# Performance work log

Hardware: AMD Instinct MI355X
Metric: run time of the kernel (lower is better)

## Reference

```python
import jax, jax.numpy as jnp
import numpy as np

D_MODEL = 256
D_STATE = 16
D_INNER = 512          # expand=2 * d_model
D_CONV = 4
DT_RANK = 16           # ceil(d_model/16)
B, L = 16, 2048


def setup_inputs() -> dict:
    key = jax.random.key(0)
    ks = jax.random.split(key, 10)
    s = 0.02
    inp = {
        "x": jax.random.normal(ks[0], (B, L, D_MODEL), dtype=jnp.float32),
        "ln_w": jnp.ones((D_MODEL,), jnp.float32),
        "ln_b": jnp.zeros((D_MODEL,), jnp.float32),
        "in_proj_w": jax.random.normal(ks[1], (2 * D_INNER, D_MODEL)) * s,
        "conv_w": jax.random.normal(ks[2], (D_INNER, 1, D_CONV)) * s,
        "conv_b": jnp.zeros((D_INNER,), jnp.float32),
        "x_proj_w": jax.random.normal(ks[3], (DT_RANK + 2 * D_STATE, D_INNER)) * s,
        "dt_proj_w": jax.random.normal(ks[4], (D_INNER, DT_RANK)) * s,
        "dt_proj_b": jax.random.uniform(ks[5], (D_INNER,), minval=-4.0, maxval=-2.0),
        "A_log": jnp.log(jnp.broadcast_to(jnp.arange(1, D_STATE + 1, dtype=jnp.float32), (D_INNER, D_STATE))).copy(),
        "D_param": jnp.ones((D_INNER,), jnp.float32),
        "out_proj_w": jax.random.normal(ks[6], (D_MODEL, D_INNER)) * s,
    }
    return inp


def _layernorm(x, w, b, eps=1e-5):
    mu = jnp.mean(x, axis=-1, keepdims=True)
    var = jnp.var(x, axis=-1, keepdims=True)
    return (x - mu) * jax.lax.rsqrt(var + eps) * w + b


def _mamba(xn, in_proj_w, conv_w, conv_b, x_proj_w, dt_proj_w, dt_proj_b, A_log, D_param, out_proj_w):
    # in_proj -> x, z   (B, L, d_inner) each
    xz = jnp.einsum('bld,ed->ble', xn, in_proj_w)
    x_in, z = jnp.split(xz, 2, axis=-1)

    # depthwise causal conv over L
    xc = jax.lax.conv_general_dilated(
        jnp.transpose(x_in, (0, 2, 1)), conv_w,
        window_strides=(1,), padding=[(D_CONV - 1, 0)],
        feature_group_count=D_INNER,
        dimension_numbers=('NCH', 'OIH', 'NCH')) + conv_b[None, :, None]
    xc = jax.nn.silu(jnp.transpose(xc, (0, 2, 1)))  # (B, L, d_inner)

    # input-dependent dt, B, C
    dbc = jnp.einsum('ble,fe->blf', xc, x_proj_w)  # (B, L, dt_rank + 2N)
    dt = jax.nn.softplus(jnp.einsum('blr,er->ble', dbc[..., :DT_RANK], dt_proj_w) + dt_proj_b)
    Bc = dbc[..., DT_RANK:DT_RANK + D_STATE]   # (B, L, N)
    Cc = dbc[..., DT_RANK + D_STATE:]          # (B, L, N)

    A = -jnp.exp(A_log)  # (d_inner, N)

    def step(h, inputs):
        dt_t, x_t, B_t, C_t = inputs  # (B,e), (B,e), (B,n), (B,n)
        dA = jnp.exp(dt_t[..., None] * A)                      # (B, e, n)
        h = dA * h + dt_t[..., None] * B_t[:, None, :] * x_t[..., None]
        y = jnp.sum(h * C_t[:, None, :], axis=-1)              # (B, e)
        return h, y

    h0 = jnp.zeros((xn.shape[0], D_INNER, D_STATE), xn.dtype)
    seq = (jnp.swapaxes(dt, 0, 1), jnp.swapaxes(xc, 0, 1),
           jnp.swapaxes(Bc, 0, 1), jnp.swapaxes(Cc, 0, 1))
    _, ys = jax.lax.scan(step, h0, seq)
    y = jnp.swapaxes(ys, 0, 1) + D_param * xc                  # (B, L, e)
    y = y * jax.nn.silu(z)
    return jnp.einsum('ble,de->bld', y, out_proj_w)


def reference(x, ln_w, ln_b, in_proj_w, conv_w, conv_b, x_proj_w, dt_proj_w, dt_proj_b, A_log, D_param, out_proj_w):
    xn = _layernorm(x, ln_w, ln_b)
    out = _mamba(xn, in_proj_w, conv_w, conv_b, x_proj_w, dt_proj_w, dt_proj_b, A_log, D_param, out_proj_w)
    return x + out  # dropout is identity in eval
```

## Files before the change

### kernel.cpp

```cpp
#include <hip/hip_runtime.h>
#include <cstdint>

#define DEVI __device__ __forceinline__

typedef __bf16 bf16;
typedef __bf16 bf16x8 __attribute__((ext_vector_type(8)));
typedef __bf16 bf16x4 __attribute__((ext_vector_type(4)));
typedef __bf16 bf16x2 __attribute__((ext_vector_type(2)));
typedef float floatx4 __attribute__((ext_vector_type(4)));
typedef float f32x2 __attribute__((ext_vector_type(2)));

constexpr int BATCH = 16, SEQ = 2048, DM = 256, DI = 512;
constexpr int M = BATCH * SEQ;
constexpr int NC = 64;
constexpr int CL = SEQ / NC;
static_assert(NC * CL == SEQ, "chunking");
constexpr float LOG2E = 1.4426950408889634f;

DEVI void gl2lds16(const void* g, void* l) {
  __builtin_amdgcn_global_load_lds(
      (const __attribute__((address_space(1))) unsigned int*)(uintptr_t)g,
      (__attribute__((address_space(3))) unsigned int*)(unsigned int)(uintptr_t)l,
      16, 0, 0);
}

DEVI float sigmoidf_(float x) { return 1.f / (1.f + __expf(-x)); }
DEVI float exp2_(float x) { return __builtin_amdgcn_exp2f(x); }

DEVI float bflo(unsigned u) { return __uint_as_float(u << 16); }
DEVI float bfhi(unsigned u) { return __uint_as_float(u & 0xFFFF0000u); }
DEVI f32x2 sp2(float v) { f32x2 r; r[0] = v; r[1] = v; return r; }

DEVI void powseq(f32x2 d, f32x2* P) {
  P[0] = d;
  P[1] = d * d;
  P[2] = P[1] * d;
  P[3] = P[1] * P[1];
  P[4] = P[3] * d;
  P[5] = P[3] * P[1];
  P[6] = P[3] * P[2];
  P[7] = P[3] * P[3];
  P[8] = P[7] * d;
  P[9] = P[7] * P[1];
  P[10] = P[7] * P[2];
  P[11] = P[7] * P[3];
  P[12] = P[7] * P[4];
  P[13] = P[7] * P[5];
  P[14] = P[7] * P[6];
  P[15] = P[7] * P[7];
}

__global__ __launch_bounds__(256) void prep_kernel(
    const float* __restrict__ w1, const float* __restrict__ wx,
    const float* __restrict__ wo, const float* __restrict__ alog,
    bf16* __restrict__ w1b, bf16* __restrict__ wxb, bf16* __restrict__ wob,
    float* __restrict__ An, int* __restrict__ flags) {
  constexpr int n1 = 1024 * 256, n2 = 48 * 512, n3 = 256 * 512;
  int i = blockIdx.x * 256 + threadIdx.x;
  if (i < n1) w1b[i] = (bf16)w1[i];
  else if (i < n1 + n2) wxb[i - n1] = (bf16)wx[i - n1];
  else if (i < n1 + n2 + n3) wob[i - n1 - n2] = (bf16)wo[i - n1 - n2];
  else if (i < n1 + n2 + n3 + DI) {
    const int e = i - (n1 + n2 + n3);
    const float a0 = -__expf(alog[e * 16]);
    bool ok = (a0 < 0.f);
#pragma unroll 1
    for (int s = 0; s < 16; s++) {
      const float a = -__expf(alog[e * 16 + s]);
      An[e * 16 + s] = a * LOG2E;
      ok = ok && (__builtin_fabsf(a / a0 - (float)(s + 1)) < 1e-3f);
    }
    flags[e] = ok ? 1 : 0;
  }
}

__global__ __launch_bounds__(256) void ln_kernel(
    const float* __restrict__ x, const float* __restrict__ w,
    const float* __restrict__ b, bf16* __restrict__ xn) {
  const int row = blockIdx.x * 4 + (threadIdx.x >> 6);
  const int lane = threadIdx.x & 63;
  const float4 v = ((const float4*)(x + (size_t)row * DM))[lane];
  float s = v.x + v.y + v.z + v.w;
  float s2 = v.x * v.x + v.y * v.y + v.z * v.z + v.w * v.w;
#pragma unroll
  for (int m = 1; m < 64; m <<= 1) { s += __shfl_xor(s, m); s2 += __shfl_xor(s2, m); }
  const float mu = s * (1.f / DM);
  const float var = s2 * (1.f / DM) - mu * mu;
  const float rs = rsqrtf(var + 1e-5f);
  const float4 wv = ((const float4*)w)[lane];
  const float4 bv = ((const float4*)b)[lane];
  bf16x4 o;
  o[0] = (bf16)((v.x - mu) * rs * wv.x + bv.x);
  o[1] = (bf16)((v.y - mu) * rs * wv.y + bv.y);
  o[2] = (bf16)((v.z - mu) * rs * wv.z + bv.z);
  o[3] = (bf16)((v.w - mu) * rs * wv.w + bv.w);
  *(bf16x4*)(xn + (size_t)row * DM + lane * 4) = o;
}

template <int N, int K, bool OUT_BF16, bool RESID>
__global__ __launch_bounds__(256) void gemm_nt(const bf16* __restrict__ A,
                                               const bf16* __restrict__ W,
                                               void* __restrict__ out,
                                               const float* __restrict__ resid) {
  constexpr int BK = 32;
  __shared__ __align__(16) bf16 lA[128 * BK];
  __shared__ __align__(16) bf16 lB[128 * BK];
  const int tid = threadIdx.x;
  const int wave = tid >> 6, lane = tid & 63;
  const int bm = blockIdx.x * 128, bn = blockIdx.y * 128;
  const int wm = (wave >> 1) * 64, wn = (wave & 1) * 64;
  const int q = lane >> 4, r = lane & 15;
  floatx4 acc[4][4] = {};
  const int c0 = wave * 64 + lane;
  const int row0 = c0 >> 2, kp = (c0 & 3) * 8;
  for (int k0 = 0; k0 < K; k0 += BK) {
    gl2lds16(A + (size_t)(bm + row0) * K + k0 + kp, lA + c0 * 8);
    gl2lds16(A + (size_t)(bm + row0 + 64) * K + k0 + kp, lA + (c0 + 256) * 8);
    gl2lds16(W + (size_t)(bn + row0) * K + k0 + kp, lB + c0 * 8);
    gl2lds16(W + (size_t)(bn + row0 + 64) * K + k0 + kp, lB + (c0 + 256) * 8);
    __syncthreads();
    bf16x8 af[4], bfr[4];
#pragma unroll
    for (int i = 0; i < 4; i++) af[i] = *(const bf16x8*)&lA[(wm + i * 16 + r) * BK + q * 8];
#pragma unroll
    for (int j = 0; j < 4; j++) bfr[j] = *(const bf16x8*)&lB[(wn + j * 16 + r) * BK + q * 8];
#pragma unroll
    for (int i = 0; i < 4; i++)
#pragma unroll
      for (int j = 0; j < 4; j++)
        acc[i][j] = __builtin_amdgcn_mfma_f32_16x16x32_bf16(af[i], bfr[j], acc[i][j], 0, 0, 0);
    __syncthreads();
  }
#pragma unroll
  for (int i = 0; i < 4; i++)
#pragma unroll
    for (int j = 0; j < 4; j++)
#pragma unroll
      for (int t = 0; t < 4; t++) {
        const int row = bm + wm + i * 16 + q * 4 + t;
        const int col = bn + wn + j * 16 + r;
        const size_t idx = (size_t)row * N + col;
        float v = acc[i][j][t];
        if constexpr (OUT_BF16) {
          ((bf16*)out)[idx] = (bf16)v;
        } else {
          if constexpr (RESID) v += resid[idx];
          ((float*)out)[idx] = v;
        }
      }
}

__global__ __launch_bounds__(256) void conv_silu(const bf16* __restrict__ xz,
                                                 const float* __restrict__ cw,
                                                 const float* __restrict__ cb,
                                                 bf16* __restrict__ xc) {
  const int tid = threadIdx.x;
  const int e2 = tid * 2;
  const int p0 = blockIdx.x * 8;
  const int b = blockIdx.y;
  const float4 w0 = ((const float4*)cw)[e2];
  const float4 w1 = ((const float4*)cw)[e2 + 1];
  const float2 bias = *(const float2*)(cb + e2);
  float xa[11], xb_[11];
#pragma unroll
  for (int j = 0; j < 11; j++) {
    const int pos = p0 - 3 + j;
    float fa = 0.f, fb = 0.f;
    if (pos >= 0) {
      const unsigned u = *(const unsigned*)(xz + ((size_t)b * SEQ + pos) * 1024 + e2);
      fa = __uint_as_float(u << 16);
      fb = __uint_as_float(u & 0xFFFF0000u);
    }
    xa[j] = fa; xb_[j] = fb;
  }
#pragma unroll
  for (int k = 0; k < 8; k++) {
    const float a0 = bias.x + xa[k] * w0.x + xa[k + 1] * w0.y + xa[k + 2] * w0.z + xa[k + 3] * w0.w;
    const float a1 = bias.y + xb_[k] * w1.x + xb_[k + 1] * w1.y + xb_[k + 2] * w1.z + xb_[k + 3] * w1.w;
    bf16x2 o;
    o[0] = (bf16)(a0 * sigmoidf_(a0));
    o[1] = (bf16)(a1 * sigmoidf_(a1));
    *(bf16x2*)(xc + ((size_t)b * SEQ + p0 + k) * DI + e2) = o;
  }
}

__global__ __launch_bounds__(256) void gemm_xproj(const bf16* __restrict__ A,
                                                  const bf16* __restrict__ W,
                                                  float* __restrict__ out) {
  constexpr int K = DI;
  __shared__ __align__(16) bf16 lW[48 * K];
  __shared__ __align__(16) bf16 lA[64 * 32];
  const int tid = threadIdx.x;
  const int wave = tid >> 6, lane = tid & 63;
  const int bm = blockIdx.x * 64;
  const int q = lane >> 4, r = lane & 15;
#pragma unroll
  for (int rd = 0; rd < 12; rd++) {
    const int c = rd * 256 + tid;
    gl2lds16((const char*)W + (size_t)c * 16, (char*)lW + (size_t)c * 16);
  }
  const int row0 = tid >> 2, kp = (tid & 3) * 8;
  const int wm = wave * 16;
  floatx4 acc[3] = {};
  for (int k0 = 0; k0 < K; k0 += 32) {
    gl2lds16(A + (size_t)(bm + row0) * K + k0 + kp, lA + tid * 8);
    __syncthreads();
    bf16x8 af = *(const bf16x8*)&lA[(wm + r) * 32 + q * 8];
#pragma unroll
    for (int j = 0; j < 3; j++) {
      const bf16x8 bfr = *(const bf16x8*)&lW[(j * 16 + r) * K + k0 + q * 8];
      acc[j] = __builtin_amdgcn_mfma_f32_16x16x32_bf16(af, bfr, acc[j], 0, 0, 0);
    }
    __syncthreads();
  }
#pragma unroll
  for (int j = 0; j < 3; j++)
#pragma unroll
    for (int t = 0; t < 4; t++)
      out[(size_t)(bm + wm + q * 4 + t) * 48 + j * 16 + r] = acc[j][t];
}

__global__ __launch_bounds__(256) void dtproj_kernel(const float* __restrict__ dbc,
                                                     const float* __restrict__ dtw,
                                                     const float* __restrict__ dtb,
                                                     bf16* __restrict__ dt) {
  __shared__ __align__(16) float sd[64 * 16];
  const int tid = threadIdx.x;
  const int p0 = blockIdx.x * 64;
  const int e = blockIdx.y * 256 + tid;
  {
    const int rowi = tid >> 2, coli = (tid & 3) * 4;
    *(float4*)&sd[rowi * 16 + coli] = *(const float4*)(dbc + (size_t)(p0 + rowi) * 48 + coli);
  }
  float w[16];
#pragma unroll
  for (int s = 0; s < 16; s += 4) {
    float4 t4 = *(const float4*)(dtw + (size_t)e * 16 + s);
    w[s] = t4.x; w[s + 1] = t4.y; w[s + 2] = t4.z; w[s + 3] = t4.w;
  }
  const float bias = dtb[e];
  __syncthreads();
  for (int p = 0; p < 64; p++) {
    float s = bias;
#pragma unroll
    for (int r2 = 0; r2 < 16; r2++) s += sd[p * 16 + r2] * w[r2];
    const float sp = (s > 15.f) ? s : __logf(1.f + __expf(s));
    dt[(size_t)(p0 + p) * DI + e] = (bf16)sp;
  }
}

DEVI void loadg2(const char* pdt, const char* pxc, int st, unsigned* ud, unsigned* ux) {
#pragma unroll
  for (int j = 0; j < 4; j++) {
    ud[j] = *(const unsigned*)(pdt + (size_t)(st + j) * (DI * 2));
    ux[j] = *(const unsigned*)(pxc + (size_t)(st + j) * (DI * 2));
  }
}
DEVI void loadg3(const char* pdt, const char* pxc, const char* pxz, int st,
                 unsigned* ud, unsigned* ux, unsigned* uz) {
#pragma unroll
  for (int j = 0; j < 4; j++) {
    ud[j] = *(const unsigned*)(pdt + (size_t)(st + j) * (DI * 2));
    ux[j] = *(const unsigned*)(pxc + (size_t)(st + j) * (DI * 2));
    uz[j] = *(const unsigned*)(pxz + (size_t)(st + j) * 2048);
  }
}

DEVI void step1f(unsigned ud, unsigned ux, const float* bc, const f32x2 A02,
                 f32x2* h, f32x2& sdt2) {
  f32x2 dt2; dt2[0] = bflo(ud); dt2[1] = bfhi(ud);
  f32x2 xv2; xv2[0] = bflo(ux); xv2[1] = bfhi(ux);
  const f32x2 dtx2 = dt2 * xv2;
  sdt2 = sdt2 + dt2;
  const f32x2 t = dt2 * A02;
  f32x2 d; d[0] = exp2_(t[0]); d[1] = exp2_(t[1]);
  f32x2 P[16];
  powseq(d, P);
  const float4* bb = (const float4*)bc;
#pragma unroll
  for (int g = 0; g < 4; g++) {
    const float4 B4 = bb[g];
    h[4 * g + 0] = P[4 * g + 0] * h[4 * g + 0] + dtx2 * sp2(B4.x);
    h[4 * g + 1] = P[4 * g + 1] * h[4 * g + 1] + dtx2 * sp2(B4.y);
    h[4 * g + 2] = P[4 * g + 2] * h[4 * g + 2] + dtx2 * sp2(B4.z);
    h[4 * g + 3] = P[4 * g + 3] * h[4 * g + 3] + dtx2 * sp2(B4.w);
  }
}

DEVI void step3f(unsigned ud, unsigned ux, unsigned uz, const float* bc,
                 const f32x2 A02, const f32x2 Dv2, f32x2* h, bf16* yo) {
  f32x2 dt2; dt2[0] = bflo(ud); dt2[1] = bfhi(ud);
  f32x2 xv2; xv2[0] = bflo(ux); xv2[1] = bfhi(ux);
  f32x2 z2; z2[0] = bflo(uz); z2[1] = bfhi(uz);
  const f32x2 dtx2 = dt2 * xv2;
  const f32x2 t = dt2 * A02;
  f32x2 d; d[0] = exp2_(t[0]); d[1] = exp2_(t[1]);
  f32x2 P[16];
  powseq(d, P);
  const float4* bb = (const float4*)bc;
  f32x2 Yv[4];
#pragma unroll
  for (int g = 0; g < 4; g++) { Yv[g][0] = 0.f; Yv[g][1] = 0.f; }
#pragma unroll
  for (int g = 0; g < 4; g++) {
    const float4 B4 = bb[g];
    const float4 C4 = bb[4 + g];
    h[4 * g + 0] = P[4 * g + 0] * h[4 * g + 0] + dtx2 * sp2(B4.x);
    Yv[g] = Yv[g] + h[4 * g + 0] * sp2(C4.x);
    h[4 * g + 1] = P[4 * g + 1] * h[4 * g + 1] + dtx2 * sp2(B4.y);
    Yv[g] = Yv[g] + h[4 * g + 1] * sp2(C4.y);
    h[4 * g + 2] = P[4 * g + 2] * h[4 * g + 2] + dtx2 * sp2(B4.z);
    Yv[g] = Yv[g] + h[4 * g + 2] * sp2(C4.z);
    h[4 * g + 3] = P[4 * g + 3] * h[4 * g + 3] + dtx2 * sp2(B4.w);
    Yv[g] = Yv[g] + h[4 * g + 3] * sp2(C4.w);
  }
  const f32x2 Ys = (Yv[0] + Yv[1]) + (Yv[2] + Yv[3]);
  f32x2 gz; gz[0] = z2[0] * sigmoidf_(z2[0]); gz[1] = z2[1] * sigmoidf_(z2[1]);
  const f32x2 yv2 = (Ys + Dv2 * xv2) * gz;
  bf16x2 o; o[0] = (bf16)yv2[0]; o[1] = (bf16)yv2[1];
  *(bf16x2*)yo = o;
}

__global__ __launch_bounds__(256) void scan_pass1(const bf16* __restrict__ dt,
                                                  const bf16* __restrict__ xc,
                                                  const float* __restrict__ dbc,
                                                  const float* __restrict__ An,
                                                  const int* __restrict__ flags,
                                                  float* __restrict__ U,
                                                  float* __restrict__ SD) {
  __shared__ __align__(16) float sbc[CL * 16];
  const int tid = threadIdx.x;
  const int e2 = tid * 2;
  const int ch = blockIdx.x, b = blockIdx.y;
  const size_t posBase = (size_t)b * SEQ + (size_t)ch * CL;
  if (tid < CL * 4) {
    const int il = tid >> 2, f = (tid & 3) * 4;
    gl2lds16(dbc + (posBase + il) * 48 + 16 + f, (char*)sbc + tid * 16);
  }
  const int2 fl = *(const int2*)(flags + e2);
  const int fast = fl.x & fl.y;
  f32x2 h[16];
#pragma unroll
  for (int s = 0; s < 16; s++) { h[s][0] = 0.f; h[s][1] = 0.f; }
  f32x2 sdt2; sdt2[0] = 0.f; sdt2[1] = 0.f;
  f32x2 A02; A02[0] = An[(size_t)e2 * 16]; A02[1] = An[(size_t)e2 * 16 + 16];
  float Aa[16], Ab[16];
  if (!fast) {
#pragma unroll
    for (int s = 0; s < 16; s += 4) {
      float4 a4 = *(const float4*)(An + (size_t)e2 * 16 + s);
      Aa[s] = a4.x; Aa[s + 1] = a4.y; Aa[s + 2] = a4.z; Aa[s + 3] = a4.w;
      float4 b4 = *(const float4*)(An + (size_t)e2 * 16 + 16 + s);
      Ab[s] = b4.x; Ab[s + 1] = b4.y; Ab[s + 2] = b4.z; Ab[s + 3] = b4.w;
    }
  }
  const char* pdt = (const char*)(dt + posBase * DI + e2);
  const char* pxc = (const char*)(xc + posBase * DI + e2);
  if (fast) {
    unsigned udA[4], uxA[4], udB[4], uxB[4];
    loadg2(pdt, pxc, 0, udA, uxA);
    __syncthreads();
#pragma unroll 1
    for (int g0 = 0; g0 < CL; g0 += 8) {
      loadg2(pdt, pxc, g0 + 4, udB, uxB);
#pragma unroll
      for (int j = 0; j < 4; j++)
        step1f(udA[j], uxA[j], sbc + (g0 + j) * 16, A02, h, sdt2);
      int nn = g0 + 8; if (nn > CL - 4) nn = CL - 4;
      loadg2(pdt, pxc, nn, udA, uxA);
#pragma unroll
      for (int j = 0; j < 4; j++)
        step1f(udB[j], uxB[j], sbc + (g0 + 4 + j) * 16, A02, h, sdt2);
    }
  } else {
    unsigned ud = *(const unsigned*)pdt;
    unsigned ux = *(const unsigned*)pxc;
    __syncthreads();
#pragma unroll 1
    for (int il = 0; il < CL; il++) {
      const int np = (il + 1 < CL) ? (il + 1) : il;
      const unsigned nud = *(const unsigned*)(pdt + (size_t)np * DI * 2);
      const unsigned nux = *(const unsigned*)(pxc + (size_t)np * DI * 2);
      const float dta = bflo(ud), dtb_v = bfhi(ud);
      const float xa = bflo(ux), xb = bfhi(ux);
      const float dtxa = dta * xa, dtxb = dtb_v * xb;
      sdt2[0] += dta; sdt2[1] += dtb_v;
      const float* bc = sbc + il * 16;
#pragma unroll
      for (int s = 0; s < 16; s++) {
        const float bv = bc[s];
        h[s][0] = exp2_(dta * Aa[s]) * h[s][0] + dtxa * bv;
        h[s][1] = exp2_(dtb_v * Ab[s]) * h[s][1] + dtxb * bv;
      }
      ud = nud; ux = nux;
    }
  }
  float* up = U + ((size_t)(b * NC + ch) * DI + e2) * 16;
#pragma unroll
  for (int i = 0; i < 4; i++) {
    float4 o; o.x = h[4 * i][0]; o.y = h[4 * i + 1][0]; o.z = h[4 * i + 2][0]; o.w = h[4 * i + 3][0];
    ((float4*)up)[i] = o;
  }
#pragma unroll
  for (int i = 0; i < 4; i++) {
    float4 o; o.x = h[4 * i][1]; o.y = h[4 * i + 1][1]; o.z = h[4 * i + 2][1]; o.w = h[4 * i + 3][1];
    ((float4*)up)[4 + i] = o;
  }
  float2 sdo; sdo.x = sdt2[0]; sdo.y = sdt2[1];
  *(float2*)(SD + (size_t)(b * NC + ch) * DI + e2) = sdo;
}

__global__ __launch_bounds__(256) void scan_pass2(const float* __restrict__ SD,
                                                  float* U,
                                                  const float* __restrict__ An) {
  const int t = blockIdx.x * 256 + threadIdx.x;
  const int s = t & 15;
  const int e = (t >> 4) & (DI - 1);
  const int b = t >> 13;
  const float Av = An[e * 16 + s];
  const float* sdp = SD + (size_t)b * NC * DI + e;
  float* up = U + ((size_t)b * NC * DI + e) * 16 + s;
  float sA_[16], uA_[16], sB_[16], uB_[16];
#pragma unroll
  for (int j = 0; j < 16; j++) {
    sA_[j] = sdp[(size_t)j * DI];
    uA_[j] = up[(size_t)j * DI * 16];
  }
  float h = 0.f;
#pragma unroll 1
  for (int c0 = 0; c0 < NC; c0 += 32) {
#pragma unroll
    for (int j = 0; j < 16; j++) {
      sB_[j] = sdp[(size_t)(c0 + 16 + j) * DI];
      uB_[j] = up[(size_t)(c0 + 16 + j) * DI * 16];
    }
#pragma unroll
    for (int j = 0; j < 16; j++) {
      const float h0 = h;
      h = exp2_(Av * sA_[j]) * h0 + uA_[j];
      up[(size_t)(c0 + j) * DI * 16] = h0;
    }
    const int nn = (c0 + 32 < NC) ? (c0 + 32) : (NC - 16);
#pragma unroll
    for (int j = 0; j < 16; j++) {
      sA_[j] = sdp[(size_t)(nn + j) * DI];
      uA_[j] = up[(size_t)(nn + j) * DI * 16];
    }
#pragma unroll
    for (int j = 0; j < 16; j++) {
      const float h0 = h;
      h = exp2_(Av * sB_[j]) * h0 + uB_[j];
      up[(size_t)(c0 + 16 + j) * DI * 16] = h0;
    }
  }
}

__global__ __launch_bounds__(256) void scan_pass3(const bf16* __restrict__ dt,
                                                  const bf16* __restrict__ xc,
                                                  const bf16* __restrict__ xz,
                                                  const float* __restrict__ dbc,
                                                  const float* __restrict__ An,
                                                  const int* __restrict__ flags,
                                                  const float* __restrict__ H0,
                                                  const float* __restrict__ Dp,
                                                  bf16* __restrict__ yg) {
  __shared__ __align__(16) float sbc[CL * 32];
  const int tid = threadIdx.x;
  const int e2 = tid * 2;
  const int ch = blockIdx.x, b = blockIdx.y;
  const size_t posBase = (size_t)b * SEQ + (size_t)ch * CL;
  {
    const int il = tid >> 3, f = (tid & 7) * 4;
    gl2lds16(dbc + (posBase + il) * 48 + 16 + f, (char*)sbc + tid * 16);
  }
  const int2 fl = *(const int2*)(flags + e2);
  const int fast = fl.x & fl.y;
  f32x2 h[16];
  const float* hp = H0 + ((size_t)(b * NC + ch) * DI + e2) * 16;
#pragma unroll
  for (int i = 0; i < 4; i++) {
    const float4 h4 = ((const float4*)hp)[i];
    h[4 * i][0] = h4.x; h[4 * i + 1][0] = h4.y; h[4 * i + 2][0] = h4.z; h[4 * i + 3][0] = h4.w;
  }
#pragma unroll
  for (int i = 0; i < 4; i++) {
    const float4 h4 = ((const float4*)hp)[4 + i];
    h[4 * i][1] = h4.x; h[4 * i + 1][1] = h4.y; h[4 * i + 2][1] = h4.z; h[4 * i + 3][1] = h4.w;
  }
  const float2 Dv = *(const float2*)(Dp + e2);
  f32x2 Dv2; Dv2[0] = Dv.x; Dv2[1] = Dv.y;
  f32x2 A02; A02[0] = An[(size_t)e2 * 16]; A02[1] = An[(size_t)e2 * 16 + 16];
  float Aa[16], Ab[16];
  if (!fast) {
#pragma unroll
    for (int s = 0; s < 16; s += 4) {
      float4 a4 = *(const float4*)(An + (size_t)e2 * 16 + s);
      Aa[s] = a4.x; Aa[s + 1] = a4.y; Aa[s + 2] = a4.z; Aa[s + 3] = a4.w;
      float4 b4 = *(const float4*)(An + (size_t)e2 * 16 + 16 + s);
      Ab[s] = b4.x; Ab[s + 1] = b4.y; Ab[s + 2] = b4.z; Ab[s + 3] = b4.w;
    }
  }
  const char* pdt = (const char*)(dt + posBase * DI + e2);
  const char* pxc = (const char*)(xc + posBase * DI + e2);
  const char* pxz = (const char*)(xz + posBase * 1024 + DI + e2);
  bf16* yo = yg + posBase * DI + e2;
  if (fast) {
    unsigned udA[4], uxA[4], uzA[4], udB[4], uxB[4], uzB[4];
    loadg3(pdt, pxc, pxz, 0, udA, uxA, uzA);
    __syncthreads();
#pragma unroll 1
    for (int g0 = 0; g0 < CL; g0 += 8) {
      loadg3(pdt, pxc, pxz, g0 + 4, udB, uxB, uzB);
#pragma unroll
      for (int j = 0; j < 4; j++)
        step3f(udA[j], uxA[j], uzA[j], sbc + (g0 + j) * 32, A02, Dv2, h,
               yo + (size_t)(g0 + j) * DI);
      int nn = g0 + 8; if (nn > CL - 4) nn = CL - 4;
      loadg3(pdt, pxc, pxz, nn, udA, uxA, uzA);
#pragma unroll
      for (int j = 0; j < 4; j++)
        step3f(udB[j], uxB[j], uzB[j], sbc + (g0 + 4 + j) * 32, A02, Dv2, h,
               yo + (size_t)(g0 + 4 + j) * DI);
    }
  } else {
    unsigned ud = *(const unsigned*)pdt;
    unsigned ux = *(const unsigned*)pxc;
    unsigned uz = *(const unsigned*)pxz;
    __syncthreads();
#pragma unroll 1
    for (int il = 0; il < CL; il++) {
      const int np = (il + 1 < CL) ? (il + 1) : il;
      const unsigned nud = *(const unsigned*)(pdt + (size_t)np * DI * 2);
      const unsigned nux = *(const unsigned*)(pxc + (size_t)np * DI * 2);
      const unsigned nuz = *(const unsigned*)(pxz + (size_t)np * 1024 * 2);
      const size_t pos = posBase + il;
      const float dta = bflo(ud), dtb_v = bfhi(ud);
      const float xa = bflo(ux), xb = bfhi(ux);
      const float za = bflo(uz), zb = bfhi(uz);
      const float dtxa = dta * xa, dtxb = dtb_v * xb;
      const float* bc = sbc + il * 32;
      float ya = 0.f, yb = 0.f;
#pragma unroll
      for (int s = 0; s < 16; s++) {
        const float bv = bc[s], cv = bc[16 + s];
        const float ha = exp2_(dta * Aa[s]) * h[s][0] + dtxa * bv;
        const float hb = exp2_(dtb_v * Ab[s]) * h[s][1] + dtxb * bv;
        h[s][0] = ha; h[s][1] = hb;
        ya += ha * cv; yb += hb * cv;
      }
      const float yva = (ya + Dv.x * xa) * za * sigmoidf_(za);
      const float yvb = (yb + Dv.y * xb) * zb * sigmoidf_(zb);
      bf16x2 o; o[0] = (bf16)yva; o[1] = (bf16)yvb;
      *(bf16x2*)(yg + pos * DI + e2) = o;
      ud = nud; ux = nux; uz = nuz;
    }
  }
}

extern "C" void kernel_launch(void* const* d_in, const int* in_sizes, int n_in,
                              void* d_out, int out_size, void* d_ws, size_t ws_size,
                              hipStream_t stream) {
  const float* x = (const float*)d_in[0];
  const float* ln_w = (const float*)d_in[1];
  const float* ln_b = (const float*)d_in[2];
  const float* w_in = (const float*)d_in[3];
  const float* conv_w = (const float*)d_in[4];
  const float* conv_b = (const float*)d_in[5];
  const float* w_x = (const float*)d_in[6];
  const float* w_dt = (const float*)d_in[7];
  const float* b_dt = (const float*)d_in[8];
  const float* a_log = (const float*)d_in[9];
  const float* d_par = (const float*)d_in[10];
  const float* w_out = (const float*)d_in[11];

  char* ws = (char*)d_ws;
  size_t off = 0;
  auto alloc = [&](size_t bytes) {
    void* p = ws + off;
    off = (off + bytes + 255) & ~(size_t)255;
    return p;
  };
  bf16* xn = (bf16*)alloc((size_t)M * DM * 2);
  bf16* xzb = (bf16*)alloc((size_t)M * 1024 * 2);
  bf16* xcb = (bf16*)alloc((size_t)M * DI * 2);
  float* dbc = (float*)alloc((size_t)M * 48 * 4);
  bf16* dtb_ = (bf16*)alloc((size_t)M * DI * 2);
  bf16* ygb = (bf16*)alloc((size_t)M * DI * 2);
  float* U = (float*)alloc((size_t)BATCH * NC * DI * 16 * 4);
  float* SD = (float*)alloc((size_t)BATCH * NC * DI * 4);
  bf16* w1b = (bf16*)alloc(1024 * 256 * 2);
  bf16* wxb = (bf16*)alloc(48 * 512 * 2);
  bf16* wob = (bf16*)alloc(256 * 512 * 2);
  float* An = (float*)alloc(512 * 16 * 4);
  int* flags = (int*)alloc(512 * 4);

  constexpr int prep_n = 1024 * 256 + 48 * 512 + 256 * 512 + DI;
  prep_kernel<<<dim3((prep_n + 255) / 256), dim3(256), 0, stream>>>(w_in, w_x, w_out, a_log, w1b, wxb, wob, An, flags);
  ln_kernel<<<dim3(M / 4), dim3(256), 0, stream>>>(x, ln_w, ln_b, xn);
  gemm_nt<1024, 256, true, false><<<dim3(M / 128, 8), dim3(256), 0, stream>>>(xn, w1b, (void*)xzb, nullptr);
  conv_silu<<<dim3(SEQ / 8, BATCH), dim3(256), 0, stream>>>(xzb, conv_w, conv_b, xcb);
  gemm_xproj<<<dim3(M / 64), dim3(256), 0, stream>>>(xcb, wxb, dbc);
  dtproj_kernel<<<dim3(M / 64, 2), dim3(256), 0, stream>>>(dbc, w_dt, b_dt, dtb_);
  scan_pass1<<<dim3(NC, BATCH), dim3(256), 0, stream>>>(dtb_, xcb, dbc, An, flags, U, SD);
  scan_pass2<<<dim3(BATCH * DI * 16 / 256), dim3(256), 0, stream>>>(SD, U, An);
  scan_pass3<<<dim3(NC, BATCH), dim3(256), 0, stream>>>(dtb_, xcb, xzb, dbc, An, flags, U, d_par, ygb);
  gemm_nt<256, 512, false, true><<<dim3(M / 128, 2), dim3(256), 0, stream>>>(ygb, wob, d_out, x);
}
```

Before: 302.5 us.

## Fuse out_proj GEMM and residual add into scan pass3 epilogue

Scan pass3 now writes its gated y tile for a 32-position chunk into shared memory and then runs an MFMA bf16 GEMM against the out_proj weight, adding the residual and writing the final output directly. This drops the y intermediate buffer round-trip and the separate output GEMM launch. The fast-path loops of pass1 and pass3 also revert from a 4-step batched prefetch to a simple one-step-ahead prefetch. The costs are larger LDS per block (about 33KB for the y tile), lower occupancy, and weight reads from global memory repeated by every block with small M=32 tiles.

```diff
diff --git a/kernel.cpp b/kernel.cpp
--- a/kernel.cpp
+++ b/kernel.cpp
@@ -249,78 +249,6 @@
   }
 }
 
-DEVI void loadg2(const char* pdt, const char* pxc, int st, unsigned* ud, unsigned* ux) {
-#pragma unroll
-  for (int j = 0; j < 4; j++) {
-    ud[j] = *(const unsigned*)(pdt + (size_t)(st + j) * (DI * 2));
-    ux[j] = *(const unsigned*)(pxc + (size_t)(st + j) * (DI * 2));
-  }
-}
-DEVI void loadg3(const char* pdt, const char* pxc, const char* pxz, int st,
-                 unsigned* ud, unsigned* ux, unsigned* uz) {
-#pragma unroll
-  for (int j = 0; j < 4; j++) {
-    ud[j] = *(const unsigned*)(pdt + (size_t)(st + j) * (DI * 2));
-    ux[j] = *(const unsigned*)(pxc + (size_t)(st + j) * (DI * 2));
-    uz[j] = *(const unsigned*)(pxz + (size_t)(st + j) * 2048);
-  }
-}
-
-DEVI void step1f(unsigned ud, unsigned ux, const float* bc, const f32x2 A02,
-                 f32x2* h, f32x2& sdt2) {
-  f32x2 dt2; dt2[0] = bflo(ud); dt2[1] = bfhi(ud);
-  f32x2 xv2; xv2[0] = bflo(ux); xv2[1] = bfhi(ux);
-  const f32x2 dtx2 = dt2 * xv2;
-  sdt2 = sdt2 + dt2;
-  const f32x2 t = dt2 * A02;
-  f32x2 d; d[0] = exp2_(t[0]); d[1] = exp2_(t[1]);
-  f32x2 P[16];
-  powseq(d, P);
-  const float4* bb = (const float4*)bc;
-#pragma unroll
-  for (int g = 0; g < 4; g++) {
-    const float4 B4 = bb[g];
-    h[4 * g + 0] = P[4 * g + 0] * h[4 * g + 0] + dtx2 * sp2(B4.x);
-    h[4 * g + 1] = P[4 * g + 1] * h[4 * g + 1] + dtx2 * sp2(B4.y);
-    h[4 * g + 2] = P[4 * g + 2] * h[4 * g + 2] + dtx2 * sp2(B4.z);
-    h[4 * g + 3] = P[4 * g + 3] * h[4 * g + 3] + dtx2 * sp2(B4.w);
-  }
-}
-
-DEVI void step3f(unsigned ud, unsigned ux, unsigned uz, const float* bc,
-                 const f32x2 A02, const f32x2 Dv2, f32x2* h, bf16* yo) {
-  f32x2 dt2; dt2[0] = bflo(ud); dt2[1] = bfhi(ud);
-  f32x2 xv2; xv2[0] = bflo(ux); xv2[1] = bfhi(ux);
-  f32x2 z2; z2[0] = bflo(uz); z2[1] = bfhi(uz);
-  const f32x2 dtx2 = dt2 * xv2;
-  const f32x2 t = dt2 * A02;
-  f32x2 d; d[0] = exp2_(t[0]); d[1] = exp2_(t[1]);
-  f32x2 P[16];
-  powseq(d, P);
-  const float4* bb = (const float4*)bc;
-  f32x2 Yv[4];
-#pragma unroll
-  for (int g = 0; g < 4; g++) { Yv[g][0] = 0.f; Yv[g][1] = 0.f; }
-#pragma unroll
-  for (int g = 0; g < 4; g++) {
-    const float4 B4 = bb[g];
-    const float4 C4 = bb[4 + g];
-    h[4 * g + 0] = P[4 * g + 0] * h[4 * g + 0] + dtx2 * sp2(B4.x);
-    Yv[g] = Yv[g] + h[4 * g + 0] * sp2(C4.x);
-    h[4 * g + 1] = P[4 * g + 1] * h[4 * g + 1] + dtx2 * sp2(B4.y);
-    Yv[g] = Yv[g] + h[4 * g + 1] * sp2(C4.y);
-    h[4 * g + 2] = P[4 * g + 2] * h[4 * g + 2] + dtx2 * sp2(B4.z);
-    Yv[g] = Yv[g] + h[4 * g + 2] * sp2(C4.z);
-    h[4 * g + 3] = P[4 * g + 3] * h[4 * g + 3] + dtx2 * sp2(B4.w);
-    Yv[g] = Yv[g] + h[4 * g + 3] * sp2(C4.w);
-  }
-  const f32x2 Ys = (Yv[0] + Yv[1]) + (Yv[2] + Yv[3]);
-  f32x2 gz; gz[0] = z2[0] * sigmoidf_(z2[0]); gz[1] = z2[1] * sigmoidf_(z2[1]);
-  const f32x2 yv2 = (Ys + Dv2 * xv2) * gz;
-  bf16x2 o; o[0] = (bf16)yv2[0]; o[1] = (bf16)yv2[1];
-  *(bf16x2*)yo = o;
-}
-
 __global__ __launch_bounds__(256) void scan_pass1(const bf16* __restrict__ dt,
                                                   const bf16* __restrict__ xc,
                                                   const float* __restrict__ dbc,
@@ -356,26 +284,35 @@
   }
   const char* pdt = (const char*)(dt + posBase * DI + e2);
   const char* pxc = (const char*)(xc + posBase * DI + e2);
+  unsigned ud = *(const unsigned*)pdt;
+  unsigned ux = *(const unsigned*)pxc;
+  __syncthreads();
   if (fast) {
-    unsigned udA[4], uxA[4], udB[4], uxB[4];
-    loadg2(pdt, pxc, 0, udA, uxA);
-    __syncthreads();
 #pragma unroll 1
-    for (int g0 = 0; g0 < CL; g0 += 8) {
-      loadg2(pdt, pxc, g0 + 4, udB, uxB);
-#pragma unroll
-      for (int j = 0; j < 4; j++)
-        step1f(udA[j], uxA[j], sbc + (g0 + j) * 16, A02, h, sdt2);
-      int nn = g0 + 8; if (nn > CL - 4) nn = CL - 4;
-      loadg2(pdt, pxc, nn, udA, uxA);
-#pragma unroll
-      for (int j = 0; j < 4; j++)
-        step1f(udB[j], uxB[j], sbc + (g0 + 4 + j) * 16, A02, h, sdt2);
+    for (int il = 0; il < CL; il++) {
+      const int np = (il + 1 < CL) ? (il + 1) : il;
+      const unsigned nud = *(const unsigned*)(pdt + (size_t)np * DI * 2);
+      const unsigned nux = *(const unsigned*)(pxc + (size_t)np * DI * 2);
+      f32x2 dt2; dt2[0] = bflo(ud); dt2[1] = bfhi(ud);
+      f32x2 xv2; xv2[0] = bflo(ux); xv2[1] = bfhi(ux);
+      const f32x2 dtx2 = dt2 * xv2;
+      sdt2 = sdt2 + dt2;
+      const f32x2 t = dt2 * A02;
+      f32x2 d; d[0] = exp2_(t[0]); d[1] = exp2_(t[1]);
+      f32x2 P[16];
+      powseq(d, P);
+      const float4* bb = (const float4*)(sbc + il * 16);
+#pragma unroll
+      for (int g = 0; g < 4; g++) {
+        const float4 B4 = bb[g];
+        h[4 * g + 0] = P[4 * g + 0] * h[4 * g + 0] + dtx2 * sp2(B4.x);
+        h[4 * g + 1] = P[4 * g + 1] * h[4 * g + 1] + dtx2 * sp2(B4.y);
+        h[4 * g + 2] = P[4 * g + 2] * h[4 * g + 2] + dtx2 * sp2(B4.z);
+        h[4 * g + 3] = P[4 * g + 3] * h[4 * g + 3] + dtx2 * sp2(B4.w);
+      }
+      ud = nud; ux = nux;
     }
   } else {
-    unsigned ud = *(const unsigned*)pdt;
-    unsigned ux = *(const unsigned*)pxc;
-    __syncthreads();
 #pragma unroll 1
     for (int il = 0; il < CL; il++) {
       const int np = (il + 1 < CL) ? (il + 1) : il;
@@ -463,8 +400,11 @@
                                                   const int* __restrict__ flags,
                                                   const float* __restrict__ H0,
                                                   const float* __restrict__ Dp,
-                                                  bf16* __restrict__ yg) {
+                                                  const bf16* __restrict__ wob,
+                                                  const float* __restrict__ xres,
+                                                  float* __restrict__ outp) {
   __shared__ __align__(16) float sbc[CL * 32];
+  __shared__ __align__(16) bf16 yt[CL][520];
   const int tid = threadIdx.x;
   const int e2 = tid * 2;
   const int ch = blockIdx.x, b = blockIdx.y;
@@ -503,37 +443,56 @@
   const char* pdt = (const char*)(dt + posBase * DI + e2);
   const char* pxc = (const char*)(xc + posBase * DI + e2);
   const char* pxz = (const char*)(xz + posBase * 1024 + DI + e2);
-  bf16* yo = yg + posBase * DI + e2;
+  unsigned ud = *(const unsigned*)pdt;
+  unsigned ux = *(const unsigned*)pxc;
+  unsigned uz = *(const unsigned*)pxz;
+  __syncthreads();
   if (fast) {
-    unsigned udA[4], uxA[4], uzA[4], udB[4], uxB[4], uzB[4];
-    loadg3(pdt, pxc, pxz, 0, udA, uxA, uzA);
-    __syncthreads();
-#pragma unroll 1
-    for (int g0 = 0; g0 < CL; g0 += 8) {
-      loadg3(pdt, pxc, pxz, g0 + 4, udB, uxB, uzB);
-#pragma unroll
-      for (int j = 0; j < 4; j++)
-        step3f(udA[j], uxA[j], uzA[j], sbc + (g0 + j) * 32, A02, Dv2, h,
-               yo + (size_t)(g0 + j) * DI);
-      int nn = g0 + 8; if (nn > CL - 4) nn = CL - 4;
-      loadg3(pdt, pxc, pxz, nn, udA, uxA, uzA);
-#pragma unroll
-      for (int j = 0; j < 4; j++)
-        step3f(udB[j], uxB[j], uzB[j], sbc + (g0 + 4 + j) * 32, A02, Dv2, h,
-               yo + (size_t)(g0 + 4 + j) * DI);
-    }
-  } else {
-    unsigned ud = *(const unsigned*)pdt;
-    unsigned ux = *(const unsigned*)pxc;
-    unsigned uz = *(const unsigned*)pxz;
-    __syncthreads();
 #pragma unroll 1
     for (int il = 0; il < CL; il++) {
       const int np = (il + 1 < CL) ? (il + 1) : il;
       const unsigned nud = *(const unsigned*)(pdt + (size_t)np * DI * 2);
       const unsigned nux = *(const unsigned*)(pxc + (size_t)np * DI * 2);
       const unsigned nuz = *(const unsigned*)(pxz + (size_t)np * 1024 * 2);
-      const size_t pos = posBase + il;
+      f32x2 dt2; dt2[0] = bflo(ud); dt2[1] = bfhi(ud);
+      f32x2 xv2; xv2[0] = bflo(ux); xv2[1] = bfhi(ux);
+      f32x2 z2; z2[0] = bflo(uz); z2[1] = bfhi(uz);
+      const f32x2 dtx2 = dt2 * xv2;
+      const f32x2 t = dt2 * A02;
+      f32x2 d; d[0] = exp2_(t[0]); d[1] = exp2_(t[1]);
+      f32x2 P[16];
+      powseq(d, P);
+      const float4* bb = (const float4*)(sbc + il * 32);
+      f32x2 Yv[4];
+#pragma unroll
+      for (int g = 0; g < 4; g++) { Yv[g][0] = 0.f; Yv[g][1] = 0.f; }
+#pragma unroll
+      for (int g = 0; g < 4; g++) {
+        const float4 B4 = bb[g];
+        const float4 C4 = bb[4 + g];
+        h[4 * g + 0] = P[4 * g + 0] * h[4 * g + 0] + dtx2 * sp2(B4.x);
+        Yv[g] = Yv[g] + h[4 * g + 0] * sp2(C4.x);
+        h[4 * g + 1] = P[4 * g + 1] * h[4 * g + 1] + dtx2 * sp2(B4.y);
+        Yv[g] = Yv[g] + h[4 * g + 1] * sp2(C4.y);
+        h[4 * g + 2] = P[4 * g + 2] * h[4 * g + 2] + dtx2 * sp2(B4.z);
+        Yv[g] = Yv[g] + h[4 * g + 2] * sp2(C4.z);
+        h[4 * g + 3] = P[4 * g + 3] * h[4 * g + 3] + dtx2 * sp2(B4.w);
+        Yv[g] = Yv[g] + h[4 * g + 3] * sp2(C4.w);
+      }
+      const f32x2 Ys = (Yv[0] + Yv[1]) + (Yv[2] + Yv[3]);
+      f32x2 gz; gz[0] = z2[0] * sigmoidf_(z2[0]); gz[1] = z2[1] * sigmoidf_(z2[1]);
+      const f32x2 yv2 = (Ys + Dv2 * xv2) * gz;
+      bf16x2 o; o[0] = (bf16)yv2[0]; o[1] = (bf16)yv2[1];
+      *(bf16x2*)&yt[il][e2] = o;
+      ud = nud; ux = nux; uz = nuz;
+    }
+  } else {
+#pragma unroll 1
+    for (int il = 0; il < CL; il++) {
+      const int np = (il + 1 < CL) ? (il + 1) : il;
+      const unsigned nud = *(const unsigned*)(pdt + (size_t)np * DI * 2);
+      const unsigned nux = *(const unsigned*)(pxc + (size_t)np * DI * 2);
+      const unsigned nuz = *(const unsigned*)(pxz + (size_t)np * 1024 * 2);
       const float dta = bflo(ud), dtb_v = bfhi(ud);
       const float xa = bflo(ux), xb = bfhi(ux);
       const float za = bflo(uz), zb = bfhi(uz);
@@ -551,10 +510,40 @@
       const float yva = (ya + Dv.x * xa) * za * sigmoidf_(za);
       const float yvb = (yb + Dv.y * xb) * zb * sigmoidf_(zb);
       bf16x2 o; o[0] = (bf16)yva; o[1] = (bf16)yvb;
-      *(bf16x2*)(yg + pos * DI + e2) = o;
+      *(bf16x2*)&yt[il][e2] = o;
       ud = nud; ux = nux; uz = nuz;
     }
   }
+  __syncthreads();
+  const int wave = tid >> 6, lane = tid & 63;
+  const int q = lane >> 4, r = lane & 15;
+  const int wn = wave * 64;
+  floatx4 acc[2][4] = {};
+#pragma unroll
+  for (int k0 = 0; k0 < DI; k0 += 32) {
+    const bf16x8 af0 = *(const bf16x8*)&yt[r][k0 + q * 8];
+    const bf16x8 af1 = *(const bf16x8*)&yt[16 + r][k0 + q * 8];
+    bf16x8 bfr[4];
+#pragma unroll
+    for (int j = 0; j < 4; j++)
+      bfr[j] = *(const bf16x8*)(wob + (size_t)(wn + j * 16 + r) * DI + k0 + q * 8);
+#pragma unroll
+    for (int j = 0; j < 4; j++) {
+      acc[0][j] = __builtin_amdgcn_mfma_f32_16x16x32_bf16(af0, bfr[j], acc[0][j], 0, 0, 0);
+      acc[1][j] = __builtin_amdgcn_mfma_f32_16x16x32_bf16(af1, bfr[j], acc[1][j], 0, 0, 0);
+    }
+  }
+#pragma unroll
+  for (int i = 0; i < 2; i++)
+#pragma unroll
+    for (int j = 0; j < 4; j++)
+#pragma unroll
+      for (int t = 0; t < 4; t++) {
+        const int rw = i * 16 + q * 4 + t;
+        const int cl_ = wn + j * 16 + r;
+        const size_t idx = (posBase + rw) * DM + cl_;
+        outp[idx] = acc[i][j][t] + xres[idx];
+      }
 }
 
 extern "C" void kernel_launch(void* const* d_in, const int* in_sizes, int n_in,
@@ -585,7 +574,6 @@
   bf16* xcb = (bf16*)alloc((size_t)M * DI * 2);
   float* dbc = (float*)alloc((size_t)M * 48 * 4);
   bf16* dtb_ = (bf16*)alloc((size_t)M * DI * 2);
-  bf16* ygb = (bf16*)alloc((size_t)M * DI * 2);
   float* U = (float*)alloc((size_t)BATCH * NC * DI * 16 * 4);
   float* SD = (float*)alloc((size_t)BATCH * NC * DI * 4);
   bf16* w1b = (bf16*)alloc(1024 * 256 * 2);
@@ -603,6 +591,5 @@
   dtproj_kernel<<<dim3(M / 64, 2), dim3(256), 0, stream>>>(dbc, w_dt, b_dt, dtb_);
   scan_pass1<<<dim3(NC, BATCH), dim3(256), 0, stream>>>(dtb_, xcb, dbc, An, flags, U, SD);
   scan_pass2<<<dim3(BATCH * DI * 16 / 256), dim3(256), 0, stream>>>(SD, U, An);
-  scan_pass3<<<dim3(NC, BATCH), dim3(256), 0, stream>>>(dtb_, xcb, xzb, dbc, An, flags, U, d_par, ygb);
-  gemm_nt<256, 512, false, true><<<dim3(M / 128, 2), dim3(256), 0, stream>>>(ygb, wob, d_out, x);
-}
+  scan_pass3<<<dim3(NC, BATCH), dim3(256), 0, stream>>>(dtb_, xcb, xzb, dbc, An, flags, U, d_par, wob, x, (float*)d_out);
+}
```

Result: slower. 311.2 us (+2.9%).
